# Performance work log

Measured on AMD Instinct MI355X. Metric: run time of the kernel, lower is better.

The kernel has to match this reference:

```python
import jax, jax.numpy as jnp
import numpy as np

ZMAX = 92          # max atomic number in NLH table
BOHR = 0.52917721  # Bohr radius in Angstrom (au.BOHR)
ENERGY_UNIT = 1.0  # multiplier for 'Ha'
N_ATOMS = 100_000
N_EDGES = 6_400_000
TAB = (ZMAX + 1) ** 2  # 8649


def setup_inputs() -> dict:
    key = jax.random.key(0)
    k1, k2, k3, k4, k5, k6, k7 = jax.random.split(key, 7)
    species = jax.random.randint(k1, (N_ATOMS,), 0, 93, dtype=jnp.int32)
    edge_src = jax.random.randint(k2, (N_EDGES,), 0, N_ATOMS, dtype=jnp.int32)
    edge_dst = jax.random.randint(k3, (N_EDGES,), 0, N_ATOMS, dtype=jnp.int32)
    # distances kept away from zero (division by rijs)
    distances = 0.5 + 4.5 * jax.random.uniform(k4, (N_EDGES,), dtype=jnp.float32)
    switch = jax.random.uniform(k5, (N_EDGES,), dtype=jnp.float32)
    CS = jax.random.uniform(k6, (TAB, 3), dtype=jnp.float32)
    ALPHAS = jax.random.uniform(k7, (TAB, 3), dtype=jnp.float32) + 0.5
    return {"species": species, "edge_src": edge_src, "edge_dst": edge_dst,
            "distances": distances, "switch": switch, "CS": CS, "ALPHAS": ALPHAS}


def reference(species, edge_src, edge_dst, distances, switch, CS, ALPHAS):
    # pair index into (zmax+1)^2 coefficient table
    s12 = species[edge_src] + ZMAX * species[edge_dst]
    cs = CS[s12]          # [E, 3]
    alphas = ALPHAS[s12]  # [E, 3]
    Z = jnp.where(species > 0, species.astype(distances.dtype), 0.0)
    # 3-term exponential screening function
    phi = jnp.sum(cs * jnp.exp(-alphas * distances[:, None]), axis=-1)  # [E]
    ereppair = Z[edge_src] * Z[edge_dst] * phi * switch / distances
    erep_atomic = ENERGY_UNIT * 0.5 * BOHR * jax.ops.segment_sum(
        ereppair, edge_src, num_segments=species.shape[0])
    return erep_atomic
```

## Files before the change

kernel.cpp:

```cpp
#include <hip/hip_runtime.h>
#include <hip/hip_fp16.h>


#define ZMAX_C 92
#define TAB93  93
#define NTAB   (TAB93 * TAB93)
#define HALF_BOHR 0.264588605f
#define NBMAX 64
#define APB 2048
#define APB_LOG 11
#define SPLITS 16
#define TPB  1024
#define NW   (TPB / 64)
#define TPB2 256
#define EPT 8
#define BLK_EDGES (TPB * EPT)
#define SPC_CAP 122880

typedef int            ivec4 __attribute__((ext_vector_type(4)));
typedef float          fvec4 __attribute__((ext_vector_type(4)));

#if __has_builtin(__builtin_amdgcn_rcpf)
#define FAST_RCP(x) __builtin_amdgcn_rcpf(x)
#else
#define FAST_RCP(x) (1.0f / (x))
#endif

__device__ __forceinline__ float half_lo(unsigned u) {
    return __half2float(*reinterpret_cast<const __half*>(&u));
}
__device__ __forceinline__ float half_hi(unsigned u) {
    unsigned s = u >> 16;
    return __half2float(*reinterpret_cast<const __half*>(&s));
}

__global__ __launch_bounds__(TPB2) void p0_prep(
    const float* __restrict__ CS, const float* __restrict__ ALPHAS,
    const int* __restrict__ species,
    uint4* __restrict__ tab16, unsigned char* __restrict__ spc8,
    unsigned* __restrict__ cursor, unsigned* __restrict__ steal,
    float* __restrict__ out, int n_atoms, int nb)
{
    int i = blockIdx.x * TPB2 + threadIdx.x;
    if (i < NTAB) {
        int sd = i / TAB93;
        int ss = i - TAB93 * sd;
        int ref = ss + ZMAX_C * sd;
        float Z = (ss > 0 && sd > 0) ? (float)(ss * sd) : 0.0f;
        __half h[8];
        h[0] = __float2half_rn(CS[3*ref+0] * Z);
        h[1] = __float2half_rn(CS[3*ref+1] * Z);
        h[2] = __float2half_rn(CS[3*ref+2] * Z);
        h[3] = __float2half_rn(-ALPHAS[3*ref+0]);
        h[4] = __float2half_rn(-ALPHAS[3*ref+1]);
        h[5] = __float2half_rn(-ALPHAS[3*ref+2]);
        h[6] = __half(0.0f); h[7] = __half(0.0f);
        tab16[i] = *reinterpret_cast<uint4*>(h);
    }
    if (i < n_atoms) {
        spc8[i] = (unsigned char)species[i];
        out[i] = 0.0f;
    }
    if (i < nb) cursor[i] = 0u;
    if (i == 0) *steal = 0u;
}

__global__ __launch_bounds__(TPB) void p1_bin_lds(
    const int* __restrict__ edge_src, const int* __restrict__ edge_dst,
    const float* __restrict__ dist, const float* __restrict__ swt,
    const unsigned char* __restrict__ spc8, const uint4* __restrict__ tab16,
    unsigned* __restrict__ pairs, unsigned* __restrict__ cursor,
    unsigned* __restrict__ steal,
    int nb, int cap, int n_edges, int n_atoms, int nchunks)
{
    __shared__ unsigned char spcL[SPC_CAP];
    __shared__ unsigned stage[BLK_EDGES];
    __shared__ unsigned histW[NW][NBMAX];
    __shared__ unsigned hist[NBMAX];
    __shared__ unsigned lbase[NBMAX];
    __shared__ unsigned gbase[NBMAX];
    __shared__ unsigned bcast;

    int tid = threadIdx.x;
    int lane = tid & 63, wave = tid >> 6;

    {
        uint4* dv = (uint4*)spcL;
        const uint4* sv = (const uint4*)spc8;
        int n16 = (n_atoms + 15) >> 4;
        for (int i = tid; i < n16; i += TPB) dv[i] = sv[i];
    }
    __syncthreads();

    for (;;) {
        if (tid == 0) bcast = atomicAdd(steal, 1u);
        ((unsigned*)histW)[tid] = 0u;
        __syncthreads();
        int c = (int)bcast;
        if (c >= nchunks) break;

        long long wbase = (long long)c * BLK_EDGES + (long long)wave * (64 * EPT);
        unsigned meta[EPT];
        unsigned short s12r[EPT];

        float rv[EPT], wv[EPT];
        {
            long long eA = wbase + lane * 4;
            long long eB = wbase + 256 + lane * 4;
            bool fullB = (eB + 3 < (long long)n_edges);
            if (fullB) {
                fvec4 r4 = *reinterpret_cast<const fvec4*>(dist + eA);
                fvec4 w4 = *reinterpret_cast<const fvec4*>(swt + eA);
                fvec4 r5 = *reinterpret_cast<const fvec4*>(dist + eB);
                fvec4 w5 = *reinterpret_cast<const fvec4*>(swt + eB);
                #pragma unroll
                for (int k = 0; k < 4; ++k) {
                    rv[k] = r4[k];     wv[k] = w4[k];
                    rv[4 + k] = r5[k]; wv[4 + k] = w5[k];
                }
            } else {
                #pragma unroll
                for (int k = 0; k < 4; ++k) {
                    long long ea = eA + k, eb = eB + k;
                    bool va = (ea < (long long)n_edges), vb = (eb < (long long)n_edges);
                    rv[k] = va ? dist[ea] : 1.f;      wv[k] = va ? swt[ea] : 0.f;
                    rv[4 + k] = vb ? dist[eb] : 1.f;  wv[4 + k] = vb ? swt[eb] : 0.f;
                }
            }
        }
        int srcv[EPT], dstv[EPT];
        #pragma unroll
        for (int j = 0; j < EPT / 4; ++j) {
            long long e0 = wbase + j * 256 + lane * 4;
            if (e0 + 3 < (long long)n_edges) {
                ivec4 s4 = *reinterpret_cast<const ivec4*>(edge_src + e0);
                ivec4 d4 = *reinterpret_cast<const ivec4*>(edge_dst + e0);
                #pragma unroll
                for (int k = 0; k < 4; ++k) { srcv[j*4+k] = s4[k]; dstv[j*4+k] = d4[k]; }
            } else {
                #pragma unroll
                for (int k = 0; k < 4; ++k) {
                    long long e = e0 + k;
                    bool v = (e < (long long)n_edges);
                    srcv[j*4+k] = v ? edge_src[e] : 0;
                    dstv[j*4+k] = v ? edge_dst[e] : 0;
                }
            }
        }
        {
            int ssv[EPT], sdv[EPT];
            #pragma unroll
            for (int i = 0; i < EPT; ++i) ssv[i] = spcL[srcv[i]];
            #pragma unroll
            for (int i = 0; i < EPT; ++i) sdv[i] = spcL[dstv[i]];
            #pragma unroll
            for (int i = 0; i < EPT; ++i)
                s12r[i] = (unsigned short)(ssv[i] + TAB93 * sdv[i]);
        }
        uint4 tv[EPT];
        #pragma unroll
        for (int k = 0; k < EPT; ++k) tv[k] = tab16[s12r[k]];

        #pragma unroll
        for (int j = 0; j < EPT / 4; ++j) {
            long long e0 = wbase + j * 256 + lane * 4;
            #pragma unroll
            for (int k = 0; k < 4; ++k) {
                int idx = j * 4 + k;
                meta[idx] = 0u;
                if (e0 + k < (long long)n_edges) {
                    unsigned b    = (unsigned)srcv[idx] >> APB_LOG;
                    unsigned lsrc = (unsigned)srcv[idx] & (APB - 1);
                    unsigned rank = atomicAdd(&histW[wave][b], 1u);
                    meta[idx] = 0x80000000u | (rank << 17) | (b << 11) | lsrc;
                }
            }
        }
        __syncthreads();
        if (tid < 64) {
            unsigned run = 0;
            #pragma unroll
            for (int w = 0; w < NW; ++w) {
                unsigned t = histW[w][tid];
                histW[w][tid] = run;
                run += t;
            }
            unsigned tot = run;
            if (tid < nb) hist[tid] = tot;
            unsigned v = (tid < nb) ? tot : 0u;
            unsigned x = v;
            #pragma unroll
            for (int off = 1; off < 64; off <<= 1) {
                unsigned y = __shfl_up(x, off);
                if ((tid & 63) >= off) x += y;
            }
            if (tid < nb) {
                lbase[tid] = x - v;
                gbase[tid] = v ? atomicAdd(cursor + tid, v) : 0u;
            }
        }
        __syncthreads();

        #pragma unroll
        for (int idx = 0; idx < EPT; ++idx) {
            unsigned m = meta[idx];
            if (!(m & 0x80000000u)) continue;
            float c0 = half_lo(tv[idx].x), c1 = half_hi(tv[idx].x);
            float c2 = half_lo(tv[idx].y), na0 = half_hi(tv[idx].y);
            float na1 = half_lo(tv[idx].z), na2 = half_hi(tv[idx].z);
            float r = rv[idx];
            float phi = c0 * __expf(na0 * r)
                      + c1 * __expf(na1 * r)
                      + c2 * __expf(na2 * r);
            float val = HALF_BOHR * phi * wv[idx] * FAST_RCP(r);
            unsigned b = (m >> 11) & 63u;
            unsigned pos = lbase[b] + histW[wave][b] + ((m >> 17) & 0x3FFFu);
            unsigned short hb = __half_as_ushort(__float2half_rn(val));
            stage[pos] = ((m & (APB - 1)) << 16) | (unsigned)hb;
        }
        __syncthreads();
        for (int b = wave; b < nb; b += NW) {
            unsigned cnt = hist[b], lb = lbase[b], gb = gbase[b];
            unsigned* dst = pairs + (size_t)b * (size_t)cap + gb;
            for (unsigned i = lane; i < cnt; i += 64)
                if (gb + i < (unsigned)cap) dst[i] = stage[lb + i];
        }
    }
}

#define TPBF 256
#define NWF  4
#define BLKF (TPBF * EPT)
__global__ __launch_bounds__(TPBF) void p1_bin(
    const int* __restrict__ edge_src, const int* __restrict__ edge_dst,
    const float* __restrict__ dist, const float* __restrict__ swt,
    const unsigned char* __restrict__ spc8, const uint4* __restrict__ tab16,
    unsigned* __restrict__ pairs, unsigned* __restrict__ cursor,
    int nb, int cap, int n_edges)
{
    __shared__ unsigned stage[BLKF];
    __shared__ unsigned hist4[NWF][NBMAX];
    __shared__ unsigned hist[NBMAX];
    __shared__ unsigned lbase[NBMAX];
    __shared__ unsigned gbase[NBMAX];

    int tid = threadIdx.x;
    ((unsigned*)hist4)[tid] = 0u;
    __syncthreads();

    int lane = tid & 63, wave = tid >> 6;
    long long wbase = (long long)blockIdx.x * BLKF + (long long)wave * (64 * EPT);

    unsigned meta[EPT];
    unsigned short s12r[EPT];
    {
        int srcv[EPT], dstv[EPT];
        #pragma unroll
        for (int j = 0; j < EPT / 4; ++j) {
            long long e0 = wbase + j * 256 + lane * 4;
            if (e0 + 3 < (long long)n_edges) {
                ivec4 s4 = *reinterpret_cast<const ivec4*>(edge_src + e0);
                ivec4 d4 = *reinterpret_cast<const ivec4*>(edge_dst + e0);
                #pragma unroll
                for (int k = 0; k < 4; ++k) { srcv[j*4+k] = s4[k]; dstv[j*4+k] = d4[k]; }
            } else {
                #pragma unroll
                for (int k = 0; k < 4; ++k) {
                    long long e = e0 + k;
                    bool v = (e < (long long)n_edges);
                    srcv[j*4+k] = v ? edge_src[e] : 0;
                    dstv[j*4+k] = v ? edge_dst[e] : 0;
                }
            }
        }
        int ssv[EPT], sdv[EPT];
        #pragma unroll
        for (int i = 0; i < EPT; ++i) ssv[i] = spc8[srcv[i]];
        #pragma unroll
        for (int i = 0; i < EPT; ++i) sdv[i] = spc8[dstv[i]];
        #pragma unroll
        for (int j = 0; j < EPT / 4; ++j) {
            long long e0 = wbase + j * 256 + lane * 4;
            #pragma unroll
            for (int k = 0; k < 4; ++k) {
                int idx = j * 4 + k;
                s12r[idx] = (unsigned short)(ssv[idx] + TAB93 * sdv[idx]);
                meta[idx] = 0u;
                if (e0 + k < (long long)n_edges) {
                    unsigned b    = (unsigned)srcv[idx] >> APB_LOG;
                    unsigned lsrc = (unsigned)srcv[idx] & (APB - 1);
                    unsigned rank = atomicAdd(&hist4[wave][b], 1u);
                    meta[idx] = 0x80000000u | (rank << 17) | (b << 11) | lsrc;
                }
            }
        }
    }
    __syncthreads();
    if (tid < 64) {
        unsigned run = 0;
        #pragma unroll
        for (int w = 0; w < NWF; ++w) {
            unsigned t = hist4[w][tid];
            hist4[w][tid] = run;
            run += t;
        }
        unsigned tot = run;
        if (tid < nb) hist[tid] = tot;
        unsigned v = (tid < nb) ? tot : 0u;
        unsigned x = v;
        #pragma unroll
        for (int off = 1; off < 64; off <<= 1) {
            unsigned y = __shfl_up(x, off);
            if ((tid & 63) >= off) x += y;
        }
        if (tid < nb) {
            lbase[tid] = x - v;
            gbase[tid] = v ? atomicAdd(cursor + tid, v) : 0u;
        }
    }
    __syncthreads();
    {
        long long eA = wbase + lane * 4;
        long long eB = wbase + 256 + lane * 4;
        float rA[4], wA[4], rB[4], wB[4];
        bool fullB = (eB + 3 < (long long)n_edges);
        if (fullB) {
            fvec4 r4 = *reinterpret_cast<const fvec4*>(dist + eA);
            fvec4 w4 = *reinterpret_cast<const fvec4*>(swt + eA);
            fvec4 r5 = *reinterpret_cast<const fvec4*>(dist + eB);
            fvec4 w5 = *reinterpret_cast<const fvec4*>(swt + eB);
            #pragma unroll
            for (int k = 0; k < 4; ++k) {
                rA[k] = r4[k]; wA[k] = w4[k]; rB[k] = r5[k]; wB[k] = w5[k];
            }
        } else {
            #pragma unroll
            for (int k = 0; k < 4; ++k) {
                long long ea = eA + k, eb = eB + k;
                bool va = (ea < (long long)n_edges), vb = (eb < (long long)n_edges);
                rA[k] = va ? dist[ea] : 1.f;  wA[k] = va ? swt[ea] : 0.f;
                rB[k] = vb ? dist[eb] : 1.f;  wB[k] = vb ? swt[eb] : 0.f;
            }
        }
        uint4 tA[4], tB[4];
        #pragma unroll
        for (int k = 0; k < 4; ++k) tA[k] = tab16[s12r[k]];
        #pragma unroll
        for (int k = 0; k < 4; ++k) tB[k] = tab16[s12r[4 + k]];
        #pragma unroll
        for (int g = 0; g < 2; ++g) {
            const float* r = g ? rB : rA;
            const float* w = g ? wB : wA;
            const uint4* t = g ? tB : tA;
            #pragma unroll
            for (int k = 0; k < 4; ++k) {
                int idx = g * 4 + k;
                unsigned m = meta[idx];
                if (!(m & 0x80000000u)) continue;
                float c0 = half_lo(t[k].x), c1 = half_hi(t[k].x);
                float c2 = half_lo(t[k].y), na0 = half_hi(t[k].y);
                float na1 = half_lo(t[k].z), na2 = half_hi(t[k].z);
                float phi = c0 * __expf(na0 * r[k])
                          + c1 * __expf(na1 * r[k])
                          + c2 * __expf(na2 * r[k]);
                float val = HALF_BOHR * phi * w[k] * FAST_RCP(r[k]);
                unsigned b = (m >> 11) & 63u;
                unsigned pos = lbase[b] + hist4[wave][b] + ((m >> 17) & 0x3FFFu);
                unsigned short hb = __half_as_ushort(__float2half_rn(val));
                stage[pos] = ((m & (APB - 1)) << 16) | (unsigned)hb;
            }
        }
    }
    __syncthreads();
    for (int b = wave; b < nb; b += NWF) {
        unsigned cnt = hist[b], lb = lbase[b], gb = gbase[b];
        unsigned* dst = pairs + (size_t)b * (size_t)cap + gb;
        for (unsigned i = lane; i < cnt; i += 64)
            if (gb + i < (unsigned)cap) dst[i] = stage[lb + i];
    }
}

__global__ __launch_bounds__(TPB2) void p2a_reduce(
    const unsigned* __restrict__ pairs, const unsigned* __restrict__ cursor,
    float* __restrict__ out, int cap, int n_atoms)
{
    int b = blockIdx.x / SPLITS;
    int s = blockIdx.x % SPLITS;
    __shared__ float acc[APB];
    for (int i = threadIdx.x; i < APB; i += TPB2) acc[i] = 0.f;
    __syncthreads();
    unsigned cnt = cursor[b];
    if (cnt > (unsigned)cap) cnt = (unsigned)cap;
    unsigned nq = (cnt + 3u) >> 2;
    unsigned qb = (unsigned)((unsigned long long)nq * s / SPLITS);
    unsigned qe = (unsigned)((unsigned long long)nq * (s + 1) / SPLITS);
    const uint4* p4 = (const uint4*)(pairs + (size_t)b * (size_t)cap);
    for (unsigned q = qb + threadIdx.x; q < qe; q += TPB2) {
        uint4 v = p4[q];
        unsigned base = q << 2;
        if (base + 3u < cnt) {
            unsafeAtomicAdd(&acc[v.x >> 16], __half2float(__ushort_as_half((unsigned short)(v.x & 0xFFFFu))));
            unsafeAtomicAdd(&acc[v.y >> 16], __half2float(__ushort_as_half((unsigned short)(v.y & 0xFFFFu))));
            unsafeAtomicAdd(&acc[v.z >> 16], __half2float(__ushort_as_half((unsigned short)(v.z & 0xFFFFu))));
            unsafeAtomicAdd(&acc[v.w >> 16], __half2float(__ushort_as_half((unsigned short)(v.w & 0xFFFFu))));
        } else {
            unsigned vv[4] = {v.x, v.y, v.z, v.w};
            #pragma unroll
            for (int e = 0; e < 4; ++e)
                if (base + (unsigned)e < cnt)
                    unsafeAtomicAdd(&acc[vv[e] >> 16],
                        __half2float(__ushort_as_half((unsigned short)(vv[e] & 0xFFFFu))));
        }
    }
    __syncthreads();
    int abase = b * APB;
    for (int k = threadIdx.x; k < APB; k += TPB2) {
        int atom = abase + k;
        float vv = acc[k];
        if (atom < n_atoms && vv != 0.0f)
            unsafeAtomicAdd(&out[atom], vv);
    }
}

__global__ __launch_bounds__(TPB2) void erep_edges_direct(
    const int* __restrict__ edge_src, const int* __restrict__ edge_dst,
    const float* __restrict__ dist, const float* __restrict__ swt,
    const int* __restrict__ species, const float* __restrict__ CS,
    const float* __restrict__ ALPHAS, float* __restrict__ out, int n_edges)
{
    int e = blockIdx.x * TPB2 + threadIdx.x;
    if (e >= n_edges) return;
    int ss = species[edge_src[e]], sd = species[edge_dst[e]];
    int prod = ss * sd;
    if (prod == 0) return;
    int s12 = ss + ZMAX_C * sd;
    float r = dist[e];
    float phi = CS[3*s12+0] * __expf(-ALPHAS[3*s12+0] * r)
              + CS[3*s12+1] * __expf(-ALPHAS[3*s12+1] * r)
              + CS[3*s12+2] * __expf(-ALPHAS[3*s12+2] * r);
    atomicAdd(out + edge_src[e],
              HALF_BOHR * (float)prod * phi * swt[e] * FAST_RCP(r));
}

extern "C" void kernel_launch(void* const* d_in, const int* in_sizes, int n_in,
                              void* d_out, int out_size, void* d_ws, size_t ws_size,
                              hipStream_t stream)
{
    const int*   species  = (const int*)  d_in[0];
    const int*   edge_src = (const int*)  d_in[1];
    const int*   edge_dst = (const int*)  d_in[2];
    const float* dist     = (const float*)d_in[3];
    const float* swt      = (const float*)d_in[4];
    const float* CS       = (const float*)d_in[5];
    const float* ALPHAS   = (const float*)d_in[6];
    float* out = (float*)d_out;

    int n_atoms = in_sizes[0];
    int n_edges = in_sizes[1];

    int nb = (n_atoms + APB - 1) / APB;
    long long capll = (long long)n_edges / nb + (long long)n_edges / ((long long)nb * 32) + 256;
    int cap = (int)((capll + 31) & ~31LL);

    size_t pairs_sz = ((size_t)nb * (size_t)cap * 4 + 255) & ~(size_t)255;
    size_t cur_sz   = ((size_t)nb * 4 + 255) & ~(size_t)255;
    size_t tab_sz   = ((size_t)NTAB * 16 + 255) & ~(size_t)255;
    size_t spc_sz   = ((size_t)n_atoms + 255) & ~(size_t)255;
    size_t syn_sz   = 256;
    size_t need = pairs_sz + cur_sz + tab_sz + spc_sz + syn_sz;

    if (nb <= NBMAX && n_edges > 0 && ws_size >= need) {
        char* w = (char*)d_ws;
        unsigned*       pairs   = (unsigned*)w;
        unsigned*       cursor  = (unsigned*)(w + pairs_sz);
        uint4*          tab16   = (uint4*)(w + pairs_sz + cur_sz);
        unsigned char*  spc8    = (unsigned char*)(w + pairs_sz + cur_sz + tab_sz);
        unsigned*       steal   = (unsigned*)(w + pairs_sz + cur_sz + tab_sz + spc_sz);

        int pmax = n_atoms > NTAB ? n_atoms : NTAB;
        p0_prep<<<(pmax + TPB2 - 1) / TPB2, TPB2, 0, stream>>>(
            CS, ALPHAS, species, tab16, spc8, cursor, steal, out, n_atoms, nb);

        if (n_atoms <= SPC_CAP) {
            int dev = 0, ncu = 256;
            (void)hipGetDevice(&dev);
            (void)hipDeviceGetAttribute(&ncu, hipDeviceAttributeMultiprocessorCount, dev);
            int nchunks = (int)(((long long)n_edges + BLK_EDGES - 1) / BLK_EDGES);
            int G = ncu > 0 ? ncu : 256;
            if (G > nchunks) G = nchunks;
            p1_bin_lds<<<G, TPB, 0, stream>>>(
                edge_src, edge_dst, dist, swt, spc8, tab16,
                pairs, cursor, steal, nb, cap, n_edges, n_atoms, nchunks);
        } else {
            p1_bin<<<(n_edges + BLKF - 1) / BLKF, TPBF, 0, stream>>>(
                edge_src, edge_dst, dist, swt, spc8, tab16,
                pairs, cursor, nb, cap, n_edges);
        }

        p2a_reduce<<<nb * SPLITS, TPB2, 0, stream>>>(pairs, cursor, out, cap, n_atoms);
    } else {
        (void)hipMemsetAsync(d_out, 0, (size_t)out_size * sizeof(float), stream);
        erep_edges_direct<<<(n_edges + TPB2 - 1) / TPB2, TPB2, 0, stream>>>(
            edge_src, edge_dst, dist, swt, species, CS, ALPHAS, out, n_edges);
    }
}
```

Before: 210.2 us.

## Prefetch next chunk's edge streams during flush and double SPLITS

```diff
diff --git a/kernel.cpp b/kernel.cpp
--- a/kernel.cpp
+++ b/kernel.cpp
@@ -9,7 +9,7 @@
 #define NBMAX 64
 #define APB 2048
 #define APB_LOG 11
-#define SPLITS 16
+#define SPLITS 32
 #define TPB  1024
 #define NW   (TPB / 64)
 #define TPB2 256
@@ -65,6 +65,43 @@
     if (i == 0) *steal = 0u;
 }
 
+#define LOAD_STREAMS(C, RV, WV, SRCV, DSTV)                                        \
+    {                                                                              \
+        long long wb_ = (long long)(C) * BLK_EDGES + (long long)wave * (64 * EPT); \
+        long long eA_ = wb_ + lane * 4;                                            \
+        long long eB_ = wb_ + 256 + lane * 4;                                      \
+        if (eB_ + 3 < (long long)n_edges) {                                        \
+            fvec4 r4 = *reinterpret_cast<const fvec4*>(dist + eA_);                \
+            fvec4 w4 = *reinterpret_cast<const fvec4*>(swt + eA_);                 \
+            ivec4 s4 = *reinterpret_cast<const ivec4*>(edge_src + eA_);            \
+            ivec4 d4 = *reinterpret_cast<const ivec4*>(edge_dst + eA_);            \
+            fvec4 r5 = *reinterpret_cast<const fvec4*>(dist + eB_);                \
+            fvec4 w5 = *reinterpret_cast<const fvec4*>(swt + eB_);                 \
+            ivec4 s5 = *reinterpret_cast<const ivec4*>(edge_src + eB_);            \
+            ivec4 d5 = *reinterpret_cast<const ivec4*>(edge_dst + eB_);            \
+            _Pragma("unroll")                                                      \
+            for (int k_ = 0; k_ < 4; ++k_) {                                       \
+                RV[k_] = r4[k_];     WV[k_] = w4[k_];                              \
+                SRCV[k_] = s4[k_];   DSTV[k_] = d4[k_];                            \
+                RV[4+k_] = r5[k_];   WV[4+k_] = w5[k_];                            \
+                SRCV[4+k_] = s5[k_]; DSTV[4+k_] = d5[k_];                          \
+            }                                                                      \
+        } else {                                                                   \
+            _Pragma("unroll")                                                      \
+            for (int k_ = 0; k_ < 4; ++k_) {                                       \
+                long long ea_ = eA_ + k_, eb_ = eB_ + k_;                          \
+                bool va_ = (ea_ >= 0 && ea_ < (long long)n_edges);                 \
+                bool vb_ = (eb_ >= 0 && eb_ < (long long)n_edges);                 \
+                RV[k_]   = va_ ? dist[ea_] : 1.f;  WV[k_]   = va_ ? swt[ea_] : 0.f;\
+                SRCV[k_] = va_ ? edge_src[ea_] : 0;                                \
+                DSTV[k_] = va_ ? edge_dst[ea_] : 0;                                \
+                RV[4+k_]   = vb_ ? dist[eb_] : 1.f; WV[4+k_] = vb_ ? swt[eb_] : 0.f;\
+                SRCV[4+k_] = vb_ ? edge_src[eb_] : 0;                              \
+                DSTV[4+k_] = vb_ ? edge_dst[eb_] : 0;                              \
+            }                                                                      \
+        }                                                                          \
+    }
+
 __global__ __launch_bounds__(TPB) void p1_bin_lds(
     const int* __restrict__ edge_src, const int* __restrict__ edge_dst,
     const float* __restrict__ dist, const float* __restrict__ swt,
@@ -81,8 +118,14 @@
     __shared__ unsigned gbase[NBMAX];
     __shared__ unsigned bcast;
 
-    int tid = threadIdx.x;
+    int tid = threadIdx.x, bid = blockIdx.x;
+    const int G = gridDim.x;
     int lane = tid & 63, wave = tid >> 6;
+
+    int c = bid;
+    float rv[EPT], wv[EPT];
+    int srcv[EPT], dstv[EPT];
+    if (c < nchunks) LOAD_STREAMS(c, rv, wv, srcv, dstv);
 
     {
         uint4* dv = (uint4*)spcL;
@@ -90,63 +133,14 @@
         int n16 = (n_atoms + 15) >> 4;
         for (int i = tid; i < n16; i += TPB) dv[i] = sv[i];
     }
-    __syncthreads();
-
-    for (;;) {
-        if (tid == 0) bcast = atomicAdd(steal, 1u);
-        ((unsigned*)histW)[tid] = 0u;
-        __syncthreads();
-        int c = (int)bcast;
-        if (c >= nchunks) break;
-
+    ((unsigned*)histW)[tid] = 0u;
+    __syncthreads();
+
+    while (c < nchunks) {
         long long wbase = (long long)c * BLK_EDGES + (long long)wave * (64 * EPT);
         unsigned meta[EPT];
         unsigned short s12r[EPT];
 
-        float rv[EPT], wv[EPT];
-        {
-            long long eA = wbase + lane * 4;
-            long long eB = wbase + 256 + lane * 4;
-            bool fullB = (eB + 3 < (long long)n_edges);
-            if (fullB) {
-                fvec4 r4 = *reinterpret_cast<const fvec4*>(dist + eA);
-                fvec4 w4 = *reinterpret_cast<const fvec4*>(swt + eA);
-                fvec4 r5 = *reinterpret_cast<const fvec4*>(dist + eB);
-                fvec4 w5 = *reinterpret_cast<const fvec4*>(swt + eB);
-                #pragma unroll
-                for (int k = 0; k < 4; ++k) {
-                    rv[k] = r4[k];     wv[k] = w4[k];
-                    rv[4 + k] = r5[k]; wv[4 + k] = w5[k];
-                }
-            } else {
-                #pragma unroll
-                for (int k = 0; k < 4; ++k) {
-                    long long ea = eA + k, eb = eB + k;
-                    bool va = (ea < (long long)n_edges), vb = (eb < (long long)n_edges);
-                    rv[k] = va ? dist[ea] : 1.f;      wv[k] = va ? swt[ea] : 0.f;
-                    rv[4 + k] = vb ? dist[eb] : 1.f;  wv[4 + k] = vb ? swt[eb] : 0.f;
-                }
-            }
-        }
-        int srcv[EPT], dstv[EPT];
-        #pragma unroll
-        for (int j = 0; j < EPT / 4; ++j) {
-            long long e0 = wbase + j * 256 + lane * 4;
-            if (e0 + 3 < (long long)n_edges) {
-                ivec4 s4 = *reinterpret_cast<const ivec4*>(edge_src + e0);
-                ivec4 d4 = *reinterpret_cast<const ivec4*>(edge_dst + e0);
-                #pragma unroll
-                for (int k = 0; k < 4; ++k) { srcv[j*4+k] = s4[k]; dstv[j*4+k] = d4[k]; }
-            } else {
-                #pragma unroll
-                for (int k = 0; k < 4; ++k) {
-                    long long e = e0 + k;
-                    bool v = (e < (long long)n_edges);
-                    srcv[j*4+k] = v ? edge_src[e] : 0;
-                    dstv[j*4+k] = v ? edge_dst[e] : 0;
-                }
-            }
-        }
         {
             int ssv[EPT], sdv[EPT];
             #pragma unroll
@@ -177,6 +171,7 @@
             }
         }
         __syncthreads();
+        if (tid == 0) bcast = G + atomicAdd(steal, 1u);
         if (tid < 64) {
             unsigned run = 0;
             #pragma unroll
@@ -219,12 +214,19 @@
             stage[pos] = ((m & (APB - 1)) << 16) | (unsigned)hb;
         }
         __syncthreads();
+
+        int cn = (int)bcast;
+        if (cn < nchunks) LOAD_STREAMS(cn, rv, wv, srcv, dstv);
+
         for (int b = wave; b < nb; b += NW) {
             unsigned cnt = hist[b], lb = lbase[b], gb = gbase[b];
             unsigned* dst = pairs + (size_t)b * (size_t)cap + gb;
             for (unsigned i = lane; i < cnt; i += 64)
                 if (gb + i < (unsigned)cap) dst[i] = stage[lb + i];
         }
+        ((unsigned*)histW)[tid] = 0u;
+        __syncthreads();
+        c = cn;
     }
 }
 
```

After: 210.7 us. About the same (+0.3%).
